# Kernel optimization log

Hardware: AMD Instinct MI355X
Metric: run time of the kernel (lower is better)

Reference implementation:

```python
import jax, jax.numpy as jnp
import numpy as np

HIDDEN = 1024
INTER = 4096
N_EXPERTS = 8


def geglu(x, w1, w2, w3):
    # x: [N, C], w1/w2: [C, I], w3: [I, C]
    return (jax.nn.gelu(x @ w1, approximate=False) * (x @ w2)) @ w3


def setup_inputs() -> dict:
    key = jax.random.key(0)
    ks = jax.random.split(key, 8)
    s = 0.02
    x = jax.random.normal(ks[0], (2, 2048, HIDDEN), dtype=jnp.float32)
    w1s = jax.random.normal(ks[1], (HIDDEN, INTER), dtype=jnp.float32) * s
    w2s = jax.random.normal(ks[2], (HIDDEN, INTER), dtype=jnp.float32) * s
    w3s = jax.random.normal(ks[3], (INTER, HIDDEN), dtype=jnp.float32) * s
    W1 = jax.random.normal(ks[4], (N_EXPERTS, HIDDEN, INTER), dtype=jnp.float32) * s
    W2 = jax.random.normal(ks[5], (N_EXPERTS, HIDDEN, INTER), dtype=jnp.float32) * s
    W3 = jax.random.normal(ks[6], (N_EXPERTS, INTER, HIDDEN), dtype=jnp.float32) * s
    Wg = jax.random.normal(ks[7], (HIDDEN, N_EXPERTS), dtype=jnp.float32) * s
    return {"x": x, "w1s": w1s, "w2s": w2s, "w3s": w3s,
            "W1": W1, "W2": W2, "W3": W3, "Wg": Wg}


def reference(x, w1s, w2s, w3s, W1, W2, W3, Wg):
    B, T, C = x.shape
    xf = x.reshape(-1, C)  # [N, C]
    shared = geglu(xf, w1s, w2s, w3s)  # [N, C]
    logits = xf @ Wg  # [N, E]
    # top-1 of softmax == argmax of logits (softmax is monotone);
    # NOTE: original torch code does NOT multiply by the routing prob.
    idx = jnp.argmax(logits, axis=-1)  # [N]
    final = jnp.zeros_like(xf)
    for e in range(N_EXPERTS):  # small fixed expert count
        y = geglu(xf, W1[e], W2[e], W3[e])  # [N, C]
        final = final + jnp.where((idx == e)[:, None], y, 0.0)
    return (shared + final).reshape(B, T, C)
```

## Files before the change

### kernel.cpp

```cpp
#include <hip/hip_runtime.h>
#include <stdint.h>

#define HIDDEN 1024
#define INTER  4096
#define NTOK   4096
#define HROWS  (2*NTOK)
#define MAXB   72
#define NMAT   27

typedef unsigned short u16;
typedef unsigned int   u32;
typedef __bf16  bf16x8 __attribute__((ext_vector_type(8)));
typedef float   f32x4  __attribute__((ext_vector_type(4)));
typedef u32     u32x4  __attribute__((ext_vector_type(4)));

#define WAITVM(N) asm volatile("s_waitcnt vmcnt(" #N ")" ::: "memory")

__device__ __forceinline__ void hard_barrier() {
  asm volatile("" ::: "memory");
  __builtin_amdgcn_s_barrier();
  asm volatile("" ::: "memory");
}

__device__ __forceinline__ u16 f2bf(float f) {
  u32 u = __float_as_uint(f);
  u32 r = u + 0x7FFFu + ((u >> 16) & 1u);
  return (u16)(r >> 16);
}

__device__ __forceinline__ u32 cvt_pk_bf16(float lo, float hi) {
  u32 r;
  asm("v_cvt_pk_bf16_f32 %0, %1, %2" : "=v"(r) : "v"(lo), "v"(hi));
  return r;
}

__device__ __forceinline__ void glds16(const void* g, void* l) {
  __builtin_amdgcn_global_load_lds(
      (const __attribute__((address_space(1))) void*)g,
      (__attribute__((address_space(3))) void*)l, 16, 0, 0);
}


__global__ void k_init(int* cnt, int* fill) {
  if (threadIdx.x < 8) { cnt[threadIdx.x] = 0; fill[threadIdx.x] = 0; }
}

__global__ __launch_bounds__(256) void k_gate(const float* __restrict__ x,
                                              const float* __restrict__ wg,
                                              int* __restrict__ idx,
                                              int* __restrict__ cnt) {
  int wave = threadIdx.x >> 6, lane = threadIdx.x & 63;
  int t = blockIdx.x * 4 + wave;
  if (t >= NTOK) return;
  float acc[8];
  #pragma unroll
  for (int e = 0; e < 8; ++e) acc[e] = 0.f;
  const float* xr = x + (size_t)t * HIDDEN;
  for (int c = lane; c < HIDDEN; c += 64) {
    float xv = xr[c];
    const float* wrow = wg + (size_t)c * 8;
    #pragma unroll
    for (int e = 0; e < 8; ++e) acc[e] += xv * wrow[e];
  }
  #pragma unroll
  for (int e = 0; e < 8; ++e)
    for (int s = 32; s; s >>= 1) acc[e] += __shfl_xor(acc[e], s);
  if (lane == 0) {
    int best = 0; float bv = acc[0];
    #pragma unroll
    for (int e = 1; e < 8; ++e) if (acc[e] > bv) { bv = acc[e]; best = e; }
    idx[t] = best;
    atomicAdd(&cnt[best], 1);
  }
}

__global__ void k_cvt(const float* __restrict__ x, u16* __restrict__ xb, int n4) {
  int i = blockIdx.x * blockDim.x + threadIdx.x;
  if (i >= n4) return;
  float4 v = ((const float4*)x)[i];
  ushort4 o;
  o.x = f2bf(v.x); o.y = f2bf(v.y); o.z = f2bf(v.z); o.w = f2bf(v.w);
  ((ushort4*)xb)[i] = o;
}

__global__ void k_table(const int* __restrict__ cnt, int* __restrict__ off,
                        int4* __restrict__ tab, int* __restrict__ nblk) {
  if (threadIdx.x != 0 || blockIdx.x != 0) return;
  int o = 0;
  int offs[8];
  for (int e = 0; e < 8; ++e) { offs[e] = o; off[e] = o; o += cnt[e]; }
  int nb = 0;
  for (int m = 0; m < NTOK / 128; ++m)
    tab[nb++] = make_int4(8, m * 128, 128, 0);
  for (int e = 0; e < 8; ++e)
    for (int j = 0; j * 128 < cnt[e]; ++j) {
      int rows = cnt[e] - j * 128; if (rows > 128) rows = 128;
      tab[nb++] = make_int4(e, NTOK + offs[e] + j * 128, rows, offs[e] + j * 128);
    }
  *nblk = nb;
}

__global__ void k_scatter(const int* __restrict__ idx, const int* __restrict__ off,
                          int* __restrict__ fill, int* __restrict__ perm) {
  int t = blockIdx.x * blockDim.x + threadIdx.x;
  if (t >= NTOK) return;
  int e = idx[t];
  int p = atomicAdd(&fill[e], 1);
  perm[off[e] + p] = t;
}


__global__ __launch_bounds__(256) void k_wcvt(
    const float* __restrict__ w1s, const float* __restrict__ w2s,
    const float* __restrict__ w3s, const float* __restrict__ W1,
    const float* __restrict__ W2,  const float* __restrict__ W3,
    u16* __restrict__ Wb)
{
  int bid = blockIdx.x;
  int m = bid >> 9, pair = bid & 511;
  const float* src; int N, nkt, kt, pp2;
  if (m < 18) {
    N = INTER; nkt = 32;
    int mm = (m < 9) ? m : m - 9;
    const float* sp = (m < 9) ? w1s : w2s;
    const float* ep = (m < 9) ? W1 : W2;
    src = (mm == 0) ? sp : ep + (size_t)(mm - 1) * HIDDEN * INTER;
    kt = pair >> 4; pp2 = pair & 15;
  } else {
    N = HIDDEN; nkt = 128;
    int mm = m - 18;
    src = (mm == 0) ? w3s : W3 + (size_t)(mm - 1) * INTER * HIDDEN;
    kt = pair >> 2; pp2 = pair & 3;
  }

  __shared__ float tileF[32 * 256];
  int tid = threadIdx.x;
  const float* in0 = src + (size_t)(kt * 32) * N + pp2 * 256;
  #pragma unroll
  for (int i = 0; i < 8; ++i) {
    int f = tid + 256 * i;
    int k = f >> 6, c4 = f & 63;
    *(float4*)&tileF[k * 256 + c4 * 4] = *(const float4*)(in0 + (size_t)k * N + c4 * 4);
  }
  __syncthreads();

  int p2 = tid >> 7, n = tid & 127;
  int pidx = m * 1024 + (pp2 * 2 + p2) * nkt + kt;
  u16* outp = Wb + (size_t)pidx * 4096 + n * 32;
  #pragma unroll
  for (int s = 0; s < 4; ++s) {
    int k8 = s ^ ((n >> 1) & 3);
    const float* col = &tileF[(k8 * 8) * 256 + p2 * 128 + n];
    u32x4 pk;
    pk.x = cvt_pk_bf16(col[0],    col[256]);
    pk.y = cvt_pk_bf16(col[512],  col[768]);
    pk.z = cvt_pk_bf16(col[1024], col[1280]);
    pk.w = cvt_pk_bf16(col[1536], col[1792]);
    *(u32x4*)(outp + s * 8) = pk;
  }
}


#define M1_TILE(B, STG, WN)                                                          \
  do {                                                                               \
    const u16* LA = pAr  + (B) * 12288;                                              \
    const u16* L1 = pBr1 + (B) * 12288;                                              \
    const u16* L2 = pBr2 + (B) * 12288;                                              \
    if (STG) {                                                                       \
      char* Ld = smem + (((B) + 2) % 3) * 24576;                                     \
      glds16(srcA0, Ld + w * 2048);                                                  \
      glds16(srcA1, Ld + w * 2048 + 1024);                                           \
      glds16(srcB1, Ld + 8192 + w * 2048);                                           \
      glds16(srcB1 + 1024, Ld + 8192 + w * 2048 + 1024);                             \
      glds16(srcB2, Ld + 16384 + w * 2048);                                          \
      glds16(srcB2 + 1024, Ld + 16384 + w * 2048 + 1024);                            \
      srcA0 += 64; srcA1 += 64; srcB1 += 8192; srcB2 += 8192;                        \
    }                                                                                \
    bf16x8 af[4], b1[4], b2[4];                                                      \
    _Pragma("unroll")                                                                \
    for (int mi = 0; mi < 4; ++mi) af[mi] = *(const bf16x8*)(LA + mi * 512);         \
    _Pragma("unroll")                                                                \
    for (int ni = 0; ni < 4; ++ni) {                                                 \
      b1[ni] = *(const bf16x8*)(L1 + ni * 512);                                      \
      b2[ni] = *(const bf16x8*)(L2 + ni * 512);                                      \
    }                                                                                \
    __builtin_amdgcn_s_setprio(1);                                                   \
    _Pragma("unroll")                                                                \
    for (int mi = 0; mi < 4; ++mi)                                                   \
      _Pragma("unroll")                                                              \
      for (int ni = 0; ni < 4; ++ni) {                                               \
        acc1[mi][ni] = __builtin_amdgcn_mfma_f32_16x16x32_bf16(af[mi], b1[ni], acc1[mi][ni], 0, 0, 0); \
        acc2[mi][ni] = __builtin_amdgcn_mfma_f32_16x16x32_bf16(af[mi], b2[ni], acc2[mi][ni], 0, 0, 0); \
      }                                                                              \
    __builtin_amdgcn_s_setprio(0);                                                   \
    WN;                                                                              \
    hard_barrier();                                                                  \
  } while (0)

__global__ __launch_bounds__(256, 2) void k_mlp1(
    const u16* __restrict__ xb, const u16* __restrict__ Wb,
    const int* __restrict__ perm, const int4* __restrict__ tab,
    const int* __restrict__ nblk, u16* __restrict__ Hbuf)
{
  int bx = blockIdx.x;
  if (bx >= *nblk) return;
  int4 te = tab[bx];
  int g = te.x, hrow0 = te.y, rows = te.z, pb = te.w;
  int m1 = (g == 8) ? 0 : 1 + g;
  int pp = blockIdx.y;
  int nbase = pp * 128;

  extern __shared__ __align__(16) char smem[];
  int tid = threadIdx.x;
  int w = tid >> 6, lane = tid & 63;
  int q = lane >> 4, rl = lane & 15;
  int mw = w >> 1, nw = w & 1;

  int tokj[2];
  #pragma unroll
  for (int j = 0; j < 2; ++j) {
    int r = w * 32 + j * 16 + (lane >> 2);
    int rc = (r < rows) ? r : (rows - 1);
    tokj[j] = (g == 8) ? (hrow0 + rc) : perm[pb + rc];
  }
  int gch = ((lane & 3) ^ ((lane >> 3) & 3)) * 16;

  const char* srcA0 = (const char*)xb + (size_t)tokj[0] * 2048 + gch;
  const char* srcA1 = (const char*)xb + (size_t)tokj[1] * 2048 + gch;
  const char* srcB1 = (const char*)Wb + ((size_t)m1 * 1024 + pp * 32) * 8192 + w * 2048 + (lane << 4);
  const char* srcB2 = (const char*)Wb + ((size_t)(m1 + 9) * 1024 + pp * 32) * 8192 + w * 2048 + (lane << 4);

  int co = (q ^ ((rl >> 1) & 3)) * 8;
  const u16* pAr  = (const u16*)smem + (mw * 64 + rl) * 32 + co;
  const u16* pBr1 = (const u16*)smem + 4096 + (nw * 64 + rl) * 32 + co;
  const u16* pBr2 = (const u16*)smem + 8192 + (nw * 64 + rl) * 32 + co;

  f32x4 acc1[4][4], acc2[4][4];
  f32x4 z = {0.f, 0.f, 0.f, 0.f};
  #pragma unroll
  for (int mi = 0; mi < 4; ++mi)
    #pragma unroll
    for (int ni = 0; ni < 4; ++ni) { acc1[mi][ni] = z; acc2[mi][ni] = z; }

  #pragma unroll
  for (int p = 0; p < 2; ++p) {
    char* Ld = smem + p * 24576;
    glds16(srcA0, Ld + w * 2048);
    glds16(srcA1, Ld + w * 2048 + 1024);
    glds16(srcB1, Ld + 8192 + w * 2048);
    glds16(srcB1 + 1024, Ld + 8192 + w * 2048 + 1024);
    glds16(srcB2, Ld + 16384 + w * 2048);
    glds16(srcB2 + 1024, Ld + 16384 + w * 2048 + 1024);
    srcA0 += 64; srcA1 += 64; srcB1 += 8192; srcB2 += 8192;
  }
  WAITVM(6);
  hard_barrier();

  for (int r = 0; r < 10; ++r) {
    M1_TILE(0, 1, WAITVM(6));
    M1_TILE(1, 1, WAITVM(6));
    M1_TILE(2, 1, WAITVM(6));
  }
  M1_TILE(0, 0, WAITVM(0));
  M1_TILE(1, 0, (void)0);

  #pragma unroll
  for (int mi = 0; mi < 4; ++mi) {
    #pragma unroll
    for (int j = 0; j < 4; ++j) {
      int r = mw * 64 + mi * 16 + q * 4 + j;
      if (r < rows) {
        size_t hb = (size_t)(hrow0 + r) * INTER + nbase + nw * 64;
        #pragma unroll
        for (int ni = 0; ni < 4; ++ni) {
          float h1 = acc1[mi][ni][j];
          float h2 = acc2[mi][ni][j];
          float ge = 0.5f * h1 * (1.0f + erff(h1 * 0.7071067811865476f));
          Hbuf[hb + ni * 16 + rl] = f2bf(ge * h2);
        }
      }
    }
  }
}


#define M2_TILE(B, STG, WN)                                                          \
  do {                                                                               \
    const u16* LA = pAr + (B) * 8192;                                                \
    const u16* LB = pBr + (B) * 8192;                                                \
    if (STG) {                                                                       \
      char* Ld = smem + (((B) + 2) % 3) * 16384;                                     \
      glds16(srcA0, Ld + w * 2048);                                                  \
      glds16(srcA1, Ld + w * 2048 + 1024);                                           \
      glds16(srcB0, Ld + 8192 + w * 2048);                                           \
      glds16(srcB0 + 1024, Ld + 8192 + w * 2048 + 1024);                             \
      srcA0 += 64; srcA1 += 64; srcB0 += 8192;                                       \
    }                                                                                \
    bf16x8 af[4], bf[4];                                                             \
    _Pragma("unroll")                                                                \
    for (int mi = 0; mi < 4; ++mi) af[mi] = *(const bf16x8*)(LA + mi * 512);         \
    _Pragma("unroll")                                                                \
    for (int ni = 0; ni < 4; ++ni) bf[ni] = *(const bf16x8*)(LB + ni * 512);         \
    __builtin_amdgcn_s_setprio(1);                                                   \
    _Pragma("unroll")                                                                \
    for (int mi = 0; mi < 4; ++mi)                                                   \
      _Pragma("unroll")                                                              \
      for (int ni = 0; ni < 4; ++ni)                                                 \
        acc[mi][ni] = __builtin_amdgcn_mfma_f32_16x16x32_bf16(af[mi], bf[ni], acc[mi][ni], 0, 0, 0); \
    __builtin_amdgcn_s_setprio(0);                                                   \
    WN;                                                                              \
    hard_barrier();                                                                  \
  } while (0)

__global__ __launch_bounds__(256, 3) void k_mlp2(
    const u16* __restrict__ Hbuf, const u16* __restrict__ Wb,
    const int* __restrict__ perm, const int4* __restrict__ tab,
    const int* __restrict__ nblk, float* __restrict__ out,
    float* __restrict__ yexp)
{
  int bx = blockIdx.x;
  if (bx >= *nblk) return;
  int4 te = tab[bx];
  int g = te.x, hrow0 = te.y, rows = te.z, pb = te.w;
  int m3 = (g == 8) ? 18 : 19 + g;
  int pp = blockIdx.y;
  int nbase = pp * 128;

  extern __shared__ __align__(16) char smem[];
  int tid = threadIdx.x;
  int w = tid >> 6, lane = tid & 63;
  int q = lane >> 4, rl = lane & 15;
  int mw = w >> 1, nw = w & 1;

  int hr[2];
  #pragma unroll
  for (int j = 0; j < 2; ++j) {
    int r = w * 32 + j * 16 + (lane >> 2);
    int rc = (r < rows) ? r : (rows - 1);
    hr[j] = hrow0 + rc;
  }
  int gch = ((lane & 3) ^ ((lane >> 3) & 3)) * 16;

  const char* srcA0 = (const char*)Hbuf + (size_t)hr[0] * (INTER * 2) + gch;
  const char* srcA1 = (const char*)Hbuf + (size_t)hr[1] * (INTER * 2) + gch;
  const char* srcB0 = (const char*)Wb + ((size_t)m3 * 1024 + pp * 128) * 8192 + w * 2048 + (lane << 4);

  int co = (q ^ ((rl >> 1) & 3)) * 8;
  const u16* pAr = (const u16*)smem + (mw * 64 + rl) * 32 + co;
  const u16* pBr = (const u16*)smem + 4096 + (nw * 64 + rl) * 32 + co;

  f32x4 acc[4][4];
  f32x4 z = {0.f, 0.f, 0.f, 0.f};
  #pragma unroll
  for (int mi = 0; mi < 4; ++mi)
    #pragma unroll
    for (int ni = 0; ni < 4; ++ni) acc[mi][ni] = z;

  #pragma unroll
  for (int p = 0; p < 2; ++p) {
    char* Ld = smem + p * 16384;
    glds16(srcA0, Ld + w * 2048);
    glds16(srcA1, Ld + w * 2048 + 1024);
    glds16(srcB0, Ld + 8192 + w * 2048);
    glds16(srcB0 + 1024, Ld + 8192 + w * 2048 + 1024);
    srcA0 += 64; srcA1 += 64; srcB0 += 8192;
  }
  WAITVM(4);
  hard_barrier();

  for (int r = 0; r < 42; ++r) {
    M2_TILE(0, 1, WAITVM(4));
    M2_TILE(1, 1, WAITVM(4));
    M2_TILE(2, 1, WAITVM(4));
  }
  M2_TILE(0, 0, WAITVM(0));
  M2_TILE(1, 0, (void)0);

  float* dstb = (g == 8) ? out : yexp;
  #pragma unroll
  for (int mi = 0; mi < 4; ++mi) {
    #pragma unroll
    for (int j = 0; j < 4; ++j) {
      int r = mw * 64 + mi * 16 + q * 4 + j;
      if (r < rows) {
        int tok = (g == 8) ? (hrow0 + r) : perm[pb + r];
        size_t ob = (size_t)tok * HIDDEN + nbase + nw * 64;
        #pragma unroll
        for (int ni = 0; ni < 4; ++ni)
          dstb[ob + ni * 16 + rl] = acc[mi][ni][j];
      }
    }
  }
}

__global__ void k_add(float* __restrict__ out, const float* __restrict__ yexp, int n4) {
  int i = blockIdx.x * blockDim.x + threadIdx.x;
  if (i >= n4) return;
  float4 a = ((const float4*)out)[i];
  float4 b = ((const float4*)yexp)[i];
  a.x += b.x; a.y += b.y; a.z += b.z; a.w += b.w;
  ((float4*)out)[i] = a;
}


extern "C" void kernel_launch(void* const* d_in, const int* in_sizes, int n_in,
                              void* d_out, int out_size, void* d_ws, size_t ws_size,
                              hipStream_t stream) {
  const float* x   = (const float*)d_in[0];
  const float* w1s = (const float*)d_in[1];
  const float* w2s = (const float*)d_in[2];
  const float* w3s = (const float*)d_in[3];
  const float* W1  = (const float*)d_in[4];
  const float* W2  = (const float*)d_in[5];
  const float* W3  = (const float*)d_in[6];
  const float* Wg  = (const float*)d_in[7];
  float* out = (float*)d_out;

  char* ws = (char*)d_ws;
  size_t o_xb   = 0;
  size_t o_H    = o_xb   + (size_t)NTOK * HIDDEN * 2;
  size_t o_yexp = o_H    + (size_t)HROWS * INTER * 2;
  size_t o_Wb   = o_yexp + (size_t)NTOK * HIDDEN * 4;
  size_t o_idx  = o_Wb   + (size_t)NMAT * 1024 * 8192;
  size_t o_perm = o_idx  + (size_t)NTOK * 4;
  size_t o_cnt  = o_perm + (size_t)NTOK * 4;
  size_t o_off  = o_cnt  + 32;
  size_t o_fill = o_off  + 32;
  size_t o_nblk = o_fill + 32;
  size_t o_tab  = o_nblk + 32;
  size_t need   = o_tab  + (size_t)MAXB * 16;
  if (ws_size < need) return;

  u16*  xb   = (u16*)(ws + o_xb);
  u16*  Hbuf = (u16*)(ws + o_H);
  float* yexp = (float*)(ws + o_yexp);
  u16*  Wb   = (u16*)(ws + o_Wb);
  int*  idx  = (int*)(ws + o_idx);
  int*  perm = (int*)(ws + o_perm);
  int*  cnt  = (int*)(ws + o_cnt);
  int*  off  = (int*)(ws + o_off);
  int*  fill = (int*)(ws + o_fill);
  int*  nblk = (int*)(ws + o_nblk);
  int4* tab  = (int4*)(ws + o_tab);

  k_init<<<1, 64, 0, stream>>>(cnt, fill);
  k_gate<<<NTOK / 4, 256, 0, stream>>>(x, Wg, idx, cnt);
  k_cvt<<<(NTOK * HIDDEN / 4) / 256, 256, 0, stream>>>(x, xb, NTOK * HIDDEN / 4);
  k_wcvt<<<NMAT * 512, 256, 0, stream>>>(w1s, w2s, w3s, W1, W2, W3, Wb);
  k_table<<<1, 1, 0, stream>>>(cnt, off, tab, nblk);
  k_scatter<<<NTOK / 256, 256, 0, stream>>>(idx, off, fill, perm);
  k_mlp1<<<dim3(MAXB, INTER / 128), 256, 73728, stream>>>(xb, Wb, perm, tab, nblk, Hbuf);
  k_mlp2<<<dim3(MAXB, HIDDEN / 128), 256, 49152, stream>>>(Hbuf, Wb, perm, tab, nblk, out, yexp);
  k_add<<<(NTOK * HIDDEN / 4) / 256, 256, 0, stream>>>(out, yexp, NTOK * HIDDEN / 4);
}
```

Baseline: 532.1 us.

## Fuse fp32 weight conversion into GEMM staging and x conversion into gate

```diff
diff --git a/kernel.cpp b/kernel.cpp
--- a/kernel.cpp
+++ b/kernel.cpp
@@ -6,7 +6,6 @@
 #define NTOK   4096
 #define HROWS  (2*NTOK)
 #define MAXB   72
-#define NMAT   27
 
 typedef unsigned short u16;
 typedef unsigned int   u32;
@@ -48,7 +47,8 @@
 __global__ __launch_bounds__(256) void k_gate(const float* __restrict__ x,
                                               const float* __restrict__ wg,
                                               int* __restrict__ idx,
-                                              int* __restrict__ cnt) {
+                                              int* __restrict__ cnt,
+                                              u16* __restrict__ xb) {
   int wave = threadIdx.x >> 6, lane = threadIdx.x & 63;
   int t = blockIdx.x * 4 + wave;
   if (t >= NTOK) return;
@@ -56,8 +56,10 @@
   #pragma unroll
   for (int e = 0; e < 8; ++e) acc[e] = 0.f;
   const float* xr = x + (size_t)t * HIDDEN;
+  u16* xbr = xb + (size_t)t * HIDDEN;
   for (int c = lane; c < HIDDEN; c += 64) {
     float xv = xr[c];
+    xbr[c] = f2bf(xv);
     const float* wrow = wg + (size_t)c * 8;
     #pragma unroll
     for (int e = 0; e < 8; ++e) acc[e] += xv * wrow[e];
@@ -72,15 +74,6 @@
     idx[t] = best;
     atomicAdd(&cnt[best], 1);
   }
-}
-
-__global__ void k_cvt(const float* __restrict__ x, u16* __restrict__ xb, int n4) {
-  int i = blockIdx.x * blockDim.x + threadIdx.x;
-  if (i >= n4) return;
-  float4 v = ((const float4*)x)[i];
-  ushort4 o;
-  o.x = f2bf(v.x); o.y = f2bf(v.y); o.z = f2bf(v.z); o.w = f2bf(v.w);
-  ((ushort4*)xb)[i] = o;
 }
 
 __global__ void k_table(const int* __restrict__ cnt, int* __restrict__ off,
@@ -110,72 +103,30 @@
 }
 
 
-__global__ __launch_bounds__(256) void k_wcvt(
-    const float* __restrict__ w1s, const float* __restrict__ w2s,
-    const float* __restrict__ w3s, const float* __restrict__ W1,
-    const float* __restrict__ W2,  const float* __restrict__ W3,
-    u16* __restrict__ Wb)
-{
-  int bid = blockIdx.x;
-  int m = bid >> 9, pair = bid & 511;
-  const float* src; int N, nkt, kt, pp2;
-  if (m < 18) {
-    N = INTER; nkt = 32;
-    int mm = (m < 9) ? m : m - 9;
-    const float* sp = (m < 9) ? w1s : w2s;
-    const float* ep = (m < 9) ? W1 : W2;
-    src = (mm == 0) ? sp : ep + (size_t)(mm - 1) * HIDDEN * INTER;
-    kt = pair >> 4; pp2 = pair & 15;
-  } else {
-    N = HIDDEN; nkt = 128;
-    int mm = m - 18;
-    src = (mm == 0) ? w3s : W3 + (size_t)(mm - 1) * INTER * HIDDEN;
-    kt = pair >> 2; pp2 = pair & 3;
-  }
-
-  __shared__ float tileF[32 * 256];
-  int tid = threadIdx.x;
-  const float* in0 = src + (size_t)(kt * 32) * N + pp2 * 256;
-  #pragma unroll
-  for (int i = 0; i < 8; ++i) {
-    int f = tid + 256 * i;
-    int k = f >> 6, c4 = f & 63;
-    *(float4*)&tileF[k * 256 + c4 * 4] = *(const float4*)(in0 + (size_t)k * N + c4 * 4);
-  }
-  __syncthreads();
-
-  int p2 = tid >> 7, n = tid & 127;
-  int pidx = m * 1024 + (pp2 * 2 + p2) * nkt + kt;
-  u16* outp = Wb + (size_t)pidx * 4096 + n * 32;
-  #pragma unroll
-  for (int s = 0; s < 4; ++s) {
-    int k8 = s ^ ((n >> 1) & 3);
-    const float* col = &tileF[(k8 * 8) * 256 + p2 * 128 + n];
-    u32x4 pk;
-    pk.x = cvt_pk_bf16(col[0],    col[256]);
-    pk.y = cvt_pk_bf16(col[512],  col[768]);
-    pk.z = cvt_pk_bf16(col[1024], col[1280]);
-    pk.w = cvt_pk_bf16(col[1536], col[1792]);
-    *(u32x4*)(outp + s * 8) = pk;
-  }
-}
-
-
-#define M1_TILE(B, STG, WN)                                                          \
+#define STG_ISSUE(SRC, LDW)                                                          \
+  _Pragma("unroll") for (int c = 0; c < 2; ++c)                                      \
+    _Pragma("unroll") for (int d = 0; d < 8; ++d)                                    \
+      vt[c][d] = (SRC)[(size_t)((kh * 2 + c) * 8 + d) * (LDW)];
+
+#define STG_WRITE(DST)                                                               \
+  _Pragma("unroll") for (int c = 0; c < 2; ++c) {                                    \
+    int sl = (kh * 2 + c) ^ nsw;                                                     \
+    u32x4 pk;                                                                        \
+    pk.x = cvt_pk_bf16(vt[c][0], vt[c][1]);                                          \
+    pk.y = cvt_pk_bf16(vt[c][2], vt[c][3]);                                          \
+    pk.z = cvt_pk_bf16(vt[c][4], vt[c][5]);                                          \
+    pk.w = cvt_pk_bf16(vt[c][6], vt[c][7]);                                          \
+    *(u32x4*)((u16*)(DST) + sn * 32 + sl * 8) = pk;                                  \
+  }
+
+
+#define M1_TILE(B, STG)                                                              \
   do {                                                                               \
     const u16* LA = pAr  + (B) * 12288;                                              \
     const u16* L1 = pBr1 + (B) * 12288;                                              \
     const u16* L2 = pBr2 + (B) * 12288;                                              \
-    if (STG) {                                                                       \
-      char* Ld = smem + (((B) + 2) % 3) * 24576;                                     \
-      glds16(srcA0, Ld + w * 2048);                                                  \
-      glds16(srcA1, Ld + w * 2048 + 1024);                                           \
-      glds16(srcB1, Ld + 8192 + w * 2048);                                           \
-      glds16(srcB1 + 1024, Ld + 8192 + w * 2048 + 1024);                             \
-      glds16(srcB2, Ld + 16384 + w * 2048);                                          \
-      glds16(srcB2 + 1024, Ld + 16384 + w * 2048 + 1024);                            \
-      srcA0 += 64; srcA1 += 64; srcB1 += 8192; srcB2 += 8192;                        \
-    }                                                                                \
+    char* Ld = smem + (((B) + 2) % 3) * 24576;                                       \
+    if (STG) { STG_ISSUE(sB1, INTER); }                                              \
     bf16x8 af[4], b1[4], b2[4];                                                      \
     _Pragma("unroll")                                                                \
     for (int mi = 0; mi < 4; ++mi) af[mi] = *(const bf16x8*)(LA + mi * 512);         \
@@ -183,6 +134,12 @@
     for (int ni = 0; ni < 4; ++ni) {                                                 \
       b1[ni] = *(const bf16x8*)(L1 + ni * 512);                                      \
       b2[ni] = *(const bf16x8*)(L2 + ni * 512);                                      \
+    }                                                                                \
+    if (STG) {                                                                       \
+      WAITVM(0);                                                                     \
+      STG_WRITE(Ld + 8192);                                                          \
+      sB1 += 32 * INTER;                                                             \
+      STG_ISSUE(sB2, INTER);                                                         \
     }                                                                                \
     __builtin_amdgcn_s_setprio(1);                                                   \
     _Pragma("unroll")                                                                \
@@ -193,12 +150,23 @@
         acc2[mi][ni] = __builtin_amdgcn_mfma_f32_16x16x32_bf16(af[mi], b2[ni], acc2[mi][ni], 0, 0, 0); \
       }                                                                              \
     __builtin_amdgcn_s_setprio(0);                                                   \
-    WN;                                                                              \
+    if (STG) {                                                                       \
+      WAITVM(0);                                                                     \
+      STG_WRITE(Ld + 16384);                                                         \
+      sB2 += 32 * INTER;                                                             \
+      glds16(srcA0, Ld + w * 2048);                                                  \
+      glds16(srcA1, Ld + w * 2048 + 1024);                                           \
+      srcA0 += 64; srcA1 += 64;                                                      \
+    } else {                                                                         \
+      WAITVM(0);                                                                     \
+    }                                                                                \
     hard_barrier();                                                                  \
   } while (0)
 
 __global__ __launch_bounds__(256, 2) void k_mlp1(
-    const u16* __restrict__ xb, const u16* __restrict__ Wb,
+    const u16* __restrict__ xb,
+    const float* __restrict__ w1s, const float* __restrict__ w2s,
+    const float* __restrict__ W1,  const float* __restrict__ W2,
     const int* __restrict__ perm, const int4* __restrict__ tab,
     const int* __restrict__ nblk, u16* __restrict__ Hbuf)
 {
@@ -206,7 +174,6 @@
   if (bx >= *nblk) return;
   int4 te = tab[bx];
   int g = te.x, hrow0 = te.y, rows = te.z, pb = te.w;
-  int m1 = (g == 8) ? 0 : 1 + g;
   int pp = blockIdx.y;
   int nbase = pp * 128;
 
@@ -227,8 +194,11 @@
 
   const char* srcA0 = (const char*)xb + (size_t)tokj[0] * 2048 + gch;
   const char* srcA1 = (const char*)xb + (size_t)tokj[1] * 2048 + gch;
-  const char* srcB1 = (const char*)Wb + ((size_t)m1 * 1024 + pp * 32) * 8192 + w * 2048 + (lane << 4);
-  const char* srcB2 = (const char*)Wb + ((size_t)(m1 + 9) * 1024 + pp * 32) * 8192 + w * 2048 + (lane << 4);
+
+  int sn = tid & 127, kh = tid >> 7, nsw = (sn >> 1) & 3;
+  const float* sB1 = ((g == 8) ? w1s : (W1 + (size_t)g * HIDDEN * INTER)) + nbase + sn;
+  const float* sB2 = ((g == 8) ? w2s : (W2 + (size_t)g * HIDDEN * INTER)) + nbase + sn;
+  float vt[2][8];
 
   int co = (q ^ ((rl >> 1) & 3)) * 8;
   const u16* pAr  = (const u16*)smem + (mw * 64 + rl) * 32 + co;
@@ -245,24 +215,28 @@
   #pragma unroll
   for (int p = 0; p < 2; ++p) {
     char* Ld = smem + p * 24576;
+    STG_ISSUE(sB1, INTER);
+    WAITVM(0);
+    STG_WRITE(Ld + 8192);
+    sB1 += 32 * INTER;
+    STG_ISSUE(sB2, INTER);
+    WAITVM(0);
+    STG_WRITE(Ld + 16384);
+    sB2 += 32 * INTER;
     glds16(srcA0, Ld + w * 2048);
     glds16(srcA1, Ld + w * 2048 + 1024);
-    glds16(srcB1, Ld + 8192 + w * 2048);
-    glds16(srcB1 + 1024, Ld + 8192 + w * 2048 + 1024);
-    glds16(srcB2, Ld + 16384 + w * 2048);
-    glds16(srcB2 + 1024, Ld + 16384 + w * 2048 + 1024);
-    srcA0 += 64; srcA1 += 64; srcB1 += 8192; srcB2 += 8192;
-  }
-  WAITVM(6);
+    srcA0 += 64; srcA1 += 64;
+  }
+  WAITVM(2);
   hard_barrier();
 
   for (int r = 0; r < 10; ++r) {
-    M1_TILE(0, 1, WAITVM(6));
-    M1_TILE(1, 1, WAITVM(6));
-    M1_TILE(2, 1, WAITVM(6));
-  }
-  M1_TILE(0, 0, WAITVM(0));
-  M1_TILE(1, 0, (void)0);
+    M1_TILE(0, 1);
+    M1_TILE(1, 1);
+    M1_TILE(2, 1);
+  }
+  M1_TILE(0, 0);
+  M1_TILE(1, 0);
 
   #pragma unroll
   for (int mi = 0; mi < 4; ++mi) {
@@ -284,23 +258,24 @@
 }
 
 
-#define M2_TILE(B, STG, WN)                                                          \
+#define M2_TILE(B, STG)                                                              \
   do {                                                                               \
     const u16* LA = pAr + (B) * 8192;                                                \
     const u16* LB = pBr + (B) * 8192;                                                \
+    char* Ld = smem + (((B) + 2) % 3) * 16384;                                       \
+    if (STG) { STG_ISSUE(sB3, HIDDEN); }                                             \
+    bf16x8 af[4], bf[4];                                                             \
+    _Pragma("unroll")                                                                \
+    for (int mi = 0; mi < 4; ++mi) af[mi] = *(const bf16x8*)(LA + mi * 512);         \
+    _Pragma("unroll")                                                                \
+    for (int ni = 0; ni < 4; ++ni) bf[ni] = *(const bf16x8*)(LB + ni * 512);         \
     if (STG) {                                                                       \
-      char* Ld = smem + (((B) + 2) % 3) * 16384;                                     \
-      glds16(srcA0, Ld + w * 2048);                                                  \
-      glds16(srcA1, Ld + w * 2048 + 1024);                                           \
-      glds16(srcB0, Ld + 8192 + w * 2048);                                           \
-      glds16(srcB0 + 1024, Ld + 8192 + w * 2048 + 1024);                             \
-      srcA0 += 64; srcA1 += 64; srcB0 += 8192;                                       \
+      WAITVM(0);                                                                     \
+      STG_WRITE(Ld + 8192);                                                          \
+      sB3 += 32 * HIDDEN;                                                            \
+    } else {                                                                         \
+      WAITVM(0);                                                                     \
     }                                                                                \
-    bf16x8 af[4], bf[4];                                                             \
-    _Pragma("unroll")                                                                \
-    for (int mi = 0; mi < 4; ++mi) af[mi] = *(const bf16x8*)(LA + mi * 512);         \
-    _Pragma("unroll")                                                                \
-    for (int ni = 0; ni < 4; ++ni) bf[ni] = *(const bf16x8*)(LB + ni * 512);         \
     __builtin_amdgcn_s_setprio(1);                                                   \
     _Pragma("unroll")                                                                \
     for (int mi = 0; mi < 4; ++mi)                                                   \
@@ -308,12 +283,17 @@
       for (int ni = 0; ni < 4; ++ni)                                                 \
         acc[mi][ni] = __builtin_amdgcn_mfma_f32_16x16x32_bf16(af[mi], bf[ni], acc[mi][ni], 0, 0, 0); \
     __builtin_amdgcn_s_setprio(0);                                                   \
-    WN;                                                                              \
+    if (STG) {                                                                       \
+      glds16(srcA0, Ld + w * 2048);                                                  \
+      glds16(srcA1, Ld + w * 2048 + 1024);                                           \
+      srcA0 += 64; srcA1 += 64;                                                      \
+    }                                                                                \
     hard_barrier();                                                                  \
   } while (0)
 
 __global__ __launch_bounds__(256, 3) void k_mlp2(
-    const u16* __restrict__ Hbuf, const u16* __restrict__ Wb,
+    const u16* __restrict__ Hbuf,
+    const float* __restrict__ w3s, const float* __restrict__ W3,
     const int* __restrict__ perm, const int4* __restrict__ tab,
     const int* __restrict__ nblk, float* __restrict__ out,
     float* __restrict__ yexp)
@@ -322,7 +302,6 @@
   if (bx >= *nblk) return;
   int4 te = tab[bx];
   int g = te.x, hrow0 = te.y, rows = te.z, pb = te.w;
-  int m3 = (g == 8) ? 18 : 19 + g;
   int pp = blockIdx.y;
   int nbase = pp * 128;
 
@@ -343,7 +322,10 @@
 
   const char* srcA0 = (const char*)Hbuf + (size_t)hr[0] * (INTER * 2) + gch;
   const char* srcA1 = (const char*)Hbuf + (size_t)hr[1] * (INTER * 2) + gch;
-  const char* srcB0 = (const char*)Wb + ((size_t)m3 * 1024 + pp * 128) * 8192 + w * 2048 + (lane << 4);
+
+  int sn = tid & 127, kh = tid >> 7, nsw = (sn >> 1) & 3;
+  const float* sB3 = ((g == 8) ? w3s : (W3 + (size_t)g * INTER * HIDDEN)) + nbase + sn;
+  float vt[2][8];
 
   int co = (q ^ ((rl >> 1) & 3)) * 8;
   const u16* pAr = (const u16*)smem + (mw * 64 + rl) * 32 + co;
@@ -359,22 +341,24 @@
   #pragma unroll
   for (int p = 0; p < 2; ++p) {
     char* Ld = smem + p * 16384;
+    STG_ISSUE(sB3, HIDDEN);
+    WAITVM(0);
+    STG_WRITE(Ld + 8192);
+    sB3 += 32 * HIDDEN;
     glds16(srcA0, Ld + w * 2048);
     glds16(srcA1, Ld + w * 2048 + 1024);
-    glds16(srcB0, Ld + 8192 + w * 2048);
-    glds16(srcB0 + 1024, Ld + 8192 + w * 2048 + 1024);
-    srcA0 += 64; srcA1 += 64; srcB0 += 8192;
-  }
-  WAITVM(4);
+    srcA0 += 64; srcA1 += 64;
+  }
+  WAITVM(2);
   hard_barrier();
 
   for (int r = 0; r < 42; ++r) {
-    M2_TILE(0, 1, WAITVM(4));
-    M2_TILE(1, 1, WAITVM(4));
-    M2_TILE(2, 1, WAITVM(4));
-  }
-  M2_TILE(0, 0, WAITVM(0));
-  M2_TILE(1, 0, (void)0);
+    M2_TILE(0, 1);
+    M2_TILE(1, 1);
+    M2_TILE(2, 1);
+  }
+  M2_TILE(0, 0);
+  M2_TILE(1, 0);
 
   float* dstb = (g == 8) ? out : yexp;
   #pragma unroll
@@ -420,8 +404,7 @@
   size_t o_xb   = 0;
   size_t o_H    = o_xb   + (size_t)NTOK * HIDDEN * 2;
   size_t o_yexp = o_H    + (size_t)HROWS * INTER * 2;
-  size_t o_Wb   = o_yexp + (size_t)NTOK * HIDDEN * 4;
-  size_t o_idx  = o_Wb   + (size_t)NMAT * 1024 * 8192;
+  size_t o_idx  = o_yexp + (size_t)NTOK * HIDDEN * 4;
   size_t o_perm = o_idx  + (size_t)NTOK * 4;
   size_t o_cnt  = o_perm + (size_t)NTOK * 4;
   size_t o_off  = o_cnt  + 32;
@@ -434,7 +417,6 @@
   u16*  xb   = (u16*)(ws + o_xb);
   u16*  Hbuf = (u16*)(ws + o_H);
   float* yexp = (float*)(ws + o_yexp);
-  u16*  Wb   = (u16*)(ws + o_Wb);
   int*  idx  = (int*)(ws + o_idx);
   int*  perm = (int*)(ws + o_perm);
   int*  cnt  = (int*)(ws + o_cnt);
@@ -444,12 +426,10 @@
   int4* tab  = (int4*)(ws + o_tab);
 
   k_init<<<1, 64, 0, stream>>>(cnt, fill);
-  k_gate<<<NTOK / 4, 256, 0, stream>>>(x, Wg, idx, cnt);
-  k_cvt<<<(NTOK * HIDDEN / 4) / 256, 256, 0, stream>>>(x, xb, NTOK * HIDDEN / 4);
-  k_wcvt<<<NMAT * 512, 256, 0, stream>>>(w1s, w2s, w3s, W1, W2, W3, Wb);
+  k_gate<<<NTOK / 4, 256, 0, stream>>>(x, Wg, idx, cnt, xb);
   k_table<<<1, 1, 0, stream>>>(cnt, off, tab, nblk);
   k_scatter<<<NTOK / 256, 256, 0, stream>>>(idx, off, fill, perm);
-  k_mlp1<<<dim3(MAXB, INTER / 128), 256, 73728, stream>>>(xb, Wb, perm, tab, nblk, Hbuf);
-  k_mlp2<<<dim3(MAXB, HIDDEN / 128), 256, 49152, stream>>>(Hbuf, Wb, perm, tab, nblk, out, yexp);
+  k_mlp1<<<dim3(MAXB, INTER / 128), 256, 73728, stream>>>(xb, w1s, w2s, W1, W2, perm, tab, nblk, Hbuf);
+  k_mlp2<<<dim3(MAXB, HIDDEN / 128), 256, 49152, stream>>>(Hbuf, w3s, W3, perm, tab, nblk, out, yexp);
   k_add<<<(NTOK * HIDDEN / 4) / 256, 256, 0, stream>>>(out, yexp, NTOK * HIDDEN / 4);
 }
```

Result: slower. 699.5 us (+31.5%).

## Fuse x bf16 conversion into gate kernel and XCD-swizzle GEMM block order

Applied to the files above, without the earlier changes.

```diff
diff --git a/kernel.cpp b/kernel.cpp
--- a/kernel.cpp
+++ b/kernel.cpp
@@ -40,6 +40,12 @@
       (__attribute__((address_space(3))) void*)l, 16, 0, 0);
 }
 
+__device__ __forceinline__ int xcd_swz(int orig, int T) {
+  int q = T >> 3, r = T & 7;
+  int xcd = orig & 7, pos = orig >> 3;
+  return (xcd < r ? xcd * (q + 1) : r * (q + 1) + (xcd - r) * q) + pos;
+}
+
 
 __global__ void k_init(int* cnt, int* fill) {
   if (threadIdx.x < 8) { cnt[threadIdx.x] = 0; fill[threadIdx.x] = 0; }
@@ -48,7 +54,8 @@
 __global__ __launch_bounds__(256) void k_gate(const float* __restrict__ x,
                                               const float* __restrict__ wg,
                                               int* __restrict__ idx,
-                                              int* __restrict__ cnt) {
+                                              int* __restrict__ cnt,
+                                              u16* __restrict__ xb) {
   int wave = threadIdx.x >> 6, lane = threadIdx.x & 63;
   int t = blockIdx.x * 4 + wave;
   if (t >= NTOK) return;
@@ -56,8 +63,10 @@
   #pragma unroll
   for (int e = 0; e < 8; ++e) acc[e] = 0.f;
   const float* xr = x + (size_t)t * HIDDEN;
+  u16* xbr = xb + (size_t)t * HIDDEN;
   for (int c = lane; c < HIDDEN; c += 64) {
     float xv = xr[c];
+    xbr[c] = f2bf(xv);
     const float* wrow = wg + (size_t)c * 8;
     #pragma unroll
     for (int e = 0; e < 8; ++e) acc[e] += xv * wrow[e];
@@ -72,15 +81,6 @@
     idx[t] = best;
     atomicAdd(&cnt[best], 1);
   }
-}
-
-__global__ void k_cvt(const float* __restrict__ x, u16* __restrict__ xb, int n4) {
-  int i = blockIdx.x * blockDim.x + threadIdx.x;
-  if (i >= n4) return;
-  float4 v = ((const float4*)x)[i];
-  ushort4 o;
-  o.x = f2bf(v.x); o.y = f2bf(v.y); o.z = f2bf(v.z); o.w = f2bf(v.w);
-  ((ushort4*)xb)[i] = o;
 }
 
 __global__ void k_table(const int* __restrict__ cnt, int* __restrict__ off,
@@ -202,12 +202,17 @@
     const int* __restrict__ perm, const int4* __restrict__ tab,
     const int* __restrict__ nblk, u16* __restrict__ Hbuf)
 {
-  int bx = blockIdx.x;
-  if (bx >= *nblk) return;
+  int nb = *nblk;
+  int T = nb * 32;
+  int lid = blockIdx.x;
+  if (lid >= T) return;
+  int virt = xcd_swz(lid, T);
+  int pp = virt / nb;
+  int bx = virt - pp * nb;
+
   int4 te = tab[bx];
   int g = te.x, hrow0 = te.y, rows = te.z, pb = te.w;
   int m1 = (g == 8) ? 0 : 1 + g;
-  int pp = blockIdx.y;
   int nbase = pp * 128;
 
   extern __shared__ __align__(16) char smem[];
@@ -318,12 +323,17 @@
     const int* __restrict__ nblk, float* __restrict__ out,
     float* __restrict__ yexp)
 {
-  int bx = blockIdx.x;
-  if (bx >= *nblk) return;
+  int nb = *nblk;
+  int T = nb * 8;
+  int lid = blockIdx.x;
+  if (lid >= T) return;
+  int virt = xcd_swz(lid, T);
+  int pp = virt / nb;
+  int bx = virt - pp * nb;
+
   int4 te = tab[bx];
   int g = te.x, hrow0 = te.y, rows = te.z, pb = te.w;
   int m3 = (g == 8) ? 18 : 19 + g;
-  int pp = blockIdx.y;
   int nbase = pp * 128;
 
   extern __shared__ __align__(16) char smem[];
@@ -444,12 +454,11 @@
   int4* tab  = (int4*)(ws + o_tab);
 
   k_init<<<1, 64, 0, stream>>>(cnt, fill);
-  k_gate<<<NTOK / 4, 256, 0, stream>>>(x, Wg, idx, cnt);
-  k_cvt<<<(NTOK * HIDDEN / 4) / 256, 256, 0, stream>>>(x, xb, NTOK * HIDDEN / 4);
+  k_gate<<<NTOK / 4, 256, 0, stream>>>(x, Wg, idx, cnt, xb);
   k_wcvt<<<NMAT * 512, 256, 0, stream>>>(w1s, w2s, w3s, W1, W2, W3, Wb);
   k_table<<<1, 1, 0, stream>>>(cnt, off, tab, nblk);
   k_scatter<<<NTOK / 256, 256, 0, stream>>>(idx, off, fill, perm);
-  k_mlp1<<<dim3(MAXB, INTER / 128), 256, 73728, stream>>>(xb, Wb, perm, tab, nblk, Hbuf);
-  k_mlp2<<<dim3(MAXB, HIDDEN / 128), 256, 49152, stream>>>(Hbuf, Wb, perm, tab, nblk, out, yexp);
+  k_mlp1<<<MAXB * 32, 256, 73728, stream>>>(xb, Wb, perm, tab, nblk, Hbuf);
+  k_mlp2<<<MAXB * 8, 256, 49152, stream>>>(Hbuf, Wb, perm, tab, nblk, out, yexp);
   k_add<<<(NTOK * HIDDEN / 4) / 256, 256, 0, stream>>>(out, yexp, NTOK * HIDDEN / 4);
 }
```

Measured after the change: 500.0 us. 6.0% less time.
